# Kernel tuning notes

Hardware: AMD Instinct MI355X
Metric: run time of the kernel (lower is better)

Reference implementation:

```python
import jax, jax.numpy as jnp
import numpy as np

# dims
B, L, D0, P, K = 4, 512, 640, 128, 16
C, H, NL = 32, 4, 3            # hidden channels, heads, layers
DH = C // H
RAD_IN = P + 2                 # pair feat + bppm + distance
HPT = 0.3                      # high_prob_threshold


def _build_edges(bppm, coords):
    """Backbone + kNN + high-prob edges per sample, deduped, flattened over batch."""
    src_all, dst_all = [], []
    for b in range(B):
        s_bb = np.arange(L - 1); d_bb = np.arange(1, L)
        srcs = [s_bb, d_bb]; dsts = [d_bb, s_bb]
        c = coords[b]
        d2 = ((c[:, None, :] - c[None, :, :]) ** 2).sum(-1)
        nn = np.argsort(d2, axis=1)[:, 1:K + 1]            # exclude self
        s_knn = np.repeat(np.arange(L), K); d_knn = nn.reshape(-1)
        srcs += [s_knn, d_knn]; dsts += [d_knn, s_knn]
        iu, ju = np.triu_indices(L, 2)                      # |i-j| > 1
        m = bppm[b][iu, ju] >= HPT
        hs, hd = iu[m], ju[m]
        srcs += [hs, hd]; dsts += [hd, hs]
        e = np.unique(np.stack([np.concatenate(srcs), np.concatenate(dsts)], 1), axis=0)
        src_all.append(e[:, 0] + b * L); dst_all.append(e[:, 1] + b * L)
    return np.concatenate(src_all).astype(np.int32), np.concatenate(dst_all).astype(np.int32)


def setup_inputs() -> dict:
    rng = np.random.default_rng(0)
    sequence_rep = rng.standard_normal((B, L, D0)).astype(np.float32)
    pair_rep = rng.standard_normal((B, L, L, P)).astype(np.float32)
    u = rng.random((B, L, L)).astype(np.float32)
    bppm = (0.5 * (u + u.transpose(0, 2, 1))) ** 8          # sparse-ish symmetric BPPM
    initial_coords = (10.0 * rng.standard_normal((B, L, 3))).astype(np.float32)
    edge_src, edge_dst = _build_edges(bppm, initial_coords)

    def w(*shape):
        fan = shape[-2] if len(shape) >= 2 else shape[-1]
        return (rng.standard_normal(shape) / np.sqrt(fan)).astype(np.float32)

    inp = dict(
        sequence_rep=jnp.asarray(sequence_rep), pair_rep=jnp.asarray(pair_rep),
        bppm=jnp.asarray(bppm.astype(np.float32)), initial_coords=jnp.asarray(initial_coords),
        edge_src=jnp.asarray(edge_src), edge_dst=jnp.asarray(edge_dst),
        Win0=jnp.asarray(w(D0, C)), Win1=jnp.asarray(w(1, C)),
        Wr1=jnp.asarray(w(NL, RAD_IN, 64)), br1=jnp.zeros((NL, 64), jnp.float32),
        Wr2=jnp.asarray(w(NL, 64, 4 * C)), br2=jnp.zeros((NL, 4 * C), jnp.float32),
        Wm00=jnp.asarray(w(NL, C, C)), Wm01=jnp.asarray(w(NL, C, C)),
        Wm10=jnp.asarray(w(NL, C, C)), Wm11=jnp.asarray(w(NL, C, C)),
        Wq=jnp.asarray(w(NL, C, C)), Wself0=jnp.asarray(w(NL, C, C)), Wself1=jnp.asarray(w(NL, C, C)),
        gamma0=jnp.ones((NL, C), jnp.float32), beta0=jnp.zeros((NL, C), jnp.float32),
        gamma1=jnp.ones((NL, C), jnp.float32), Wout=jnp.asarray(w(C, 1)),
    )
    return inp


def _forward(sequence_rep, pair_rep, bppm, initial_coords,
             Win0, Win1, Wr1, br1, Wr2, br2, Wm00, Wm01, Wm10, Wm11,
             Wq, Wself0, Wself1, gamma0, beta0, gamma1, Wout, edge_src, edge_dst):
    N = B * L
    x = initial_coords.reshape(N, 3)
    h0 = sequence_rep.reshape(N, D0) @ Win0                  # [N,C] degree-0
    h1 = x[:, None, :] * Win1[0][None, :, None]              # [N,C,3] degree-1
    src, dst = edge_src, edge_dst
    rel = x[dst] - x[src]
    r = jnp.sqrt(jnp.sum(rel * rel, -1) + 1e-12)             # [E]
    rhat = rel / (r[:, None] + 1e-8)                         # Y1 spherical harmonic dir
    b_idx, si, di = src // L, src % L, dst % L
    ef = jnp.concatenate([pair_rep[b_idx, si, di], bppm[b_idx, si, di][:, None], r[:, None]], -1)

    for l in range(NL):
        rad = jax.nn.relu(ef @ Wr1[l] + br1[l]) @ Wr2[l] + br2[l]   # [E,4C] radial weights
        w00, w01, w10, w11 = jnp.split(rad, 4, axis=-1)
        h0s, h1s = h0[src], h1[src]
        dot1 = jnp.einsum('ecd,ed->ec', h1s, rhat)                  # deg1 -> deg0 path
        m0 = w00 * (h0s @ Wm00[l]) + w01 * (dot1 @ Wm01[l])          # [E,C]
        m1 = (w11[:, :, None] * jnp.einsum('ecd,cf->efd', h1s, Wm11[l])
              + (w10 * (h0s @ Wm10[l]))[:, :, None] * rhat[:, None, :])  # [E,C,3]
        # multi-head attention over incoming edges
        q = (h0 @ Wq[l]).reshape(N, H, DH)
        k = m0.reshape(-1, H, DH)
        logit = jnp.sum(q[dst] * k, -1) / np.sqrt(DH)                # [E,H]
        mx = jax.ops.segment_max(logit, dst, num_segments=N)
        mx = jnp.where(jnp.isfinite(mx), mx, 0.0)
        a = jnp.exp(logit - mx[dst])
        den = jax.ops.segment_sum(a, dst, num_segments=N)
        alpha = a / (den[dst] + 1e-9)                                # [E,H]
        agg0 = jax.ops.segment_sum(alpha[:, :, None] * k, dst, num_segments=N).reshape(N, C)
        agg1 = jax.ops.segment_sum(alpha[:, :, None, None] * m1.reshape(-1, H, DH, 3),
                                   dst, num_segments=N).reshape(N, C, 3)
        h0 = h0 + agg0 @ Wself0[l]
        h1 = h1 + jnp.einsum('ncd,cf->nfd', agg1, Wself1[l])
        # norms: LayerNorm on deg-0, equivariant norm-gating on deg-1
        mu = h0.mean(-1, keepdims=True)
        h0 = (h0 - mu) / jnp.sqrt(h0.var(-1, keepdims=True) + 1e-5) * gamma0[l] + beta0[l]
        nrm = jnp.sqrt(jnp.sum(h1 * h1, -1) + 1e-12)                 # [N,C]
        nln = (nrm - nrm.mean(-1, keepdims=True)) / jnp.sqrt(nrm.var(-1, keepdims=True) + 1e-5) * gamma1[l]
        h1 = h1 * (nln / (nrm + 1e-8))[:, :, None]
    delta = jnp.einsum('ncd,co->nod', h1, Wout)[:, 0, :]             # fiber_out {'1':1}
    return (x + delta).reshape(B, L, 3)


def reference(sequence_rep, pair_rep, bppm, initial_coords, edge_src, edge_dst,
              Win0, Win1, Wr1, br1, Wr2, br2, Wm00, Wm01, Wm10, Wm11,
              Wq, Wself0, Wself1, gamma0, beta0, gamma1, Wout):
    return _forward(sequence_rep, pair_rep, bppm, initial_coords,
                    Win0, Win1, Wr1, br1, Wr2, br2, Wm00, Wm01, Wm10, Wm11,
                    Wq, Wself0, Wself1, gamma0, beta0, gamma1, Wout, edge_src, edge_dst)
```

## Files before the change

### kernel.cpp

```cpp
#include <hip/hip_runtime.h>
#include <hip/hip_bf16.h>
#include <math.h>

#define BB 4
#define LL 512
#define D0 640
#define PP 128
#define CC 32
#define NLAYER 3
#define NN (BB*LL)
#define RADIN 130

typedef __attribute__((ext_vector_type(8))) short bf16x8;
typedef __attribute__((ext_vector_type(4))) float f32x4;

__device__ __forceinline__ short f2b(float v) {
    __hip_bfloat16 h = __float2bfloat16(v);
    short s; __builtin_memcpy(&s, &h, 2); return s;
}


__global__ void k_zero_int(int* __restrict__ p, int n) {
    int i = blockIdx.x * blockDim.x + threadIdx.x;
    if (i < n) p[i] = 0;
}

__global__ __launch_bounds__(64) void k_init_h0(const float* __restrict__ seq,
                                                const float* __restrict__ Win0,
                                                float* __restrict__ h0) {
    const int n = blockIdx.x, lane = threadIdx.x;
    const int c = lane & 31, half = lane >> 5;
    const float* s = seq + (size_t)n * D0;
    float acc = 0.f;
    const int i0 = half * (D0 / 2), i1 = i0 + (D0 / 2);
    for (int i = i0; i < i1; ++i) acc = fmaf(s[i], Win0[i * CC + c], acc);
    acc += __shfl_xor(acc, 32);
    if (lane < 32) h0[n * CC + c] = acc;
}

__global__ void k_init_h1(const float* __restrict__ x, const float* __restrict__ Win1,
                          float* __restrict__ h1) {
    int idx = blockIdx.x * blockDim.x + threadIdx.x;
    if (idx >= NN * CC) return;
    int n = idx >> 5, c = idx & 31;
    float w = Win1[c];
    const float* xp = x + n * 3;
    float* hp = h1 + (size_t)n * 96 + c * 3;
    hp[0] = xp[0] * w; hp[1] = xp[1] * w; hp[2] = xp[2] * w;
}

__global__ void k_geom(const int* __restrict__ src, const int* __restrict__ dst,
                       const float* __restrict__ x, float* __restrict__ r_e,
                       float* __restrict__ rhat, int E) {
    int e = blockIdx.x * blockDim.x + threadIdx.x;
    if (e >= E) return;
    int s = src[e], d = dst[e];
    float dx = x[d * 3 + 0] - x[s * 3 + 0];
    float dy = x[d * 3 + 1] - x[s * 3 + 1];
    float dz = x[d * 3 + 2] - x[s * 3 + 2];
    float r = sqrtf(dx * dx + dy * dy + dz * dz + 1e-12f);
    float ir = 1.f / (r + 1e-8f);
    r_e[e] = r;
    rhat[e * 3 + 0] = dx * ir; rhat[e * 3 + 1] = dy * ir; rhat[e * 3 + 2] = dz * ir;
}

__global__ void k_count(const int* __restrict__ dst, int* __restrict__ deg, int E) {
    int e = blockIdx.x * blockDim.x + threadIdx.x;
    if (e < E) atomicAdd(&deg[dst[e]], 1);
}

__global__ __launch_bounds__(64) void k_scan(const int* __restrict__ deg,
                                             int* __restrict__ rowptr,
                                             int* __restrict__ cursor) {
    const int lane = threadIdx.x;
    const int base = lane * 32;
    int loc[32]; int s = 0;
    for (int i = 0; i < 32; ++i) { loc[i] = deg[base + i]; s += loc[i]; }
    int pre = s;
    for (int off = 1; off < 64; off <<= 1) {
        int t = __shfl_up(pre, off);
        if (lane >= off) pre += t;
    }
    pre -= s;
    int run = pre;
    for (int i = 0; i < 32; ++i) { rowptr[base + i] = run; cursor[base + i] = 0; run += loc[i]; }
    if (lane == 63) rowptr[NN] = run;
}

__global__ void k_scatter(const int* __restrict__ dst, const int* __restrict__ rowptr,
                          int* __restrict__ cursor, int* __restrict__ einc, int E) {
    int e = blockIdx.x * blockDim.x + threadIdx.x;
    if (e >= E) return;
    int d = dst[e];
    int pos = atomicAdd(&cursor[d], 1);
    einc[rowptr[d] + pos] = e;
}

__global__ __launch_bounds__(256) void k_build_ef(
    const int* __restrict__ src, const int* __restrict__ dst,
    const float* __restrict__ pair, const float* __restrict__ bppm,
    const float* __restrict__ r_e, short* __restrict__ efb, int E)
{
    int e = blockIdx.x * 4 + (threadIdx.x >> 6);
    int lane = threadIdx.x & 63;
    if (e >= E) return;
    int s = src[e], d = dst[e];
    int b = s / LL, si = s % LL, di = d % LL;
    size_t prow = ((size_t)b * LL + si) * LL + di;
    const float* pr = pair + prow * PP;
    short* out = efb + (size_t)e * 160;
    out[lane] = f2b(pr[lane]);
    out[64 + lane] = f2b(pr[64 + lane]);
    if (lane < 32) {
        int idx = 128 + lane;
        float v = 0.f;
        if (idx == 128) v = bppm[prow];
        else if (idx == 129) v = r_e[e];
        out[idx] = f2b(v);
    }
}

__global__ void k_pack(const float* __restrict__ Wr1, const float* __restrict__ Wr2,
                       short* __restrict__ W1p, short* __restrict__ W2p) {
    int t = blockIdx.x * blockDim.x + threadIdx.x;
    const int tot1 = NLAYER * 5 * 4 * 64 * 8;
    const int tot2 = NLAYER * 2 * 8 * 64 * 8;
    if (t < tot1) {
        int j = t & 7; int r = t >> 3;
        int ln = r & 63; r >>= 6;
        int cb = r & 3; r >>= 2;
        int kb = r % 5; int l = r / 5;
        int row = kb * 32 + (ln >> 4) * 8 + j;
        int col = cb * 16 + (ln & 15);
        float v = (row < RADIN) ? Wr1[((size_t)l * RADIN + row) * 64 + col] : 0.f;
        W1p[t] = f2b(v);
    } else if (t < tot1 + tot2) {
        int t2 = t - tot1;
        int j = t2 & 7; int r = t2 >> 3;
        int ln = r & 63; r >>= 6;
        int cb = r & 7; r >>= 3;
        int kb = r & 1; int l = r >> 1;
        int row = kb * 32 + (ln >> 4) * 8 + j;
        int col = cb * 16 + (ln & 15);
        W2p[t2] = f2b(Wr2[((size_t)l * 64 + row) * 128 + col]);
    }
}

__global__ __launch_bounds__(256) void k_nodepre(
    int l, const float* __restrict__ h0, const float* __restrict__ h1,
    const float* __restrict__ Wq, const float* __restrict__ Wm00,
    const float* __restrict__ Wm10, const float* __restrict__ Wm11,
    float* __restrict__ qbuf, float* __restrict__ P00,
    float* __restrict__ P10, float* __restrict__ P11)
{
    __shared__ float sh0[8][32], sh1[8][96];
    const int c = threadIdx.x & 31, hw = threadIdx.x >> 5;
    const int n = blockIdx.x * 8 + hw;
    sh0[hw][c] = h0[n * CC + c];
    const float* hp = h1 + (size_t)n * 96 + c * 3;
    sh1[hw][c * 3 + 0] = hp[0]; sh1[hw][c * 3 + 1] = hp[1]; sh1[hw][c * 3 + 2] = hp[2];
    const float* WqL  = Wq   + l * 1024;
    const float* W00L = Wm00 + l * 1024;
    const float* W10L = Wm10 + l * 1024;
    const float* W11L = Wm11 + l * 1024;
    float q = 0.f, p00 = 0.f, p10 = 0.f, px = 0.f, py = 0.f, pz = 0.f;
    for (int i = 0; i < 32; ++i) {
        float a = sh0[hw][i];
        q   = fmaf(a, WqL[i * 32 + c], q);
        p00 = fmaf(a, W00L[i * 32 + c], p00);
        p10 = fmaf(a, W10L[i * 32 + c], p10);
        float w = W11L[i * 32 + c];
        px = fmaf(sh1[hw][i * 3 + 0], w, px);
        py = fmaf(sh1[hw][i * 3 + 1], w, py);
        pz = fmaf(sh1[hw][i * 3 + 2], w, pz);
    }
    qbuf[n * 32 + c] = q; P00[n * 32 + c] = p00; P10[n * 32 + c] = p10;
    float* pp = P11 + (size_t)n * 96 + c * 3;
    pp[0] = px; pp[1] = py; pp[2] = pz;
}

__global__ __launch_bounds__(256) void k_radial(
    int l, int E,
    const short* __restrict__ efb,
    const short* __restrict__ W1p,
    const short* __restrict__ W2p,
    const float* __restrict__ br1,
    const float* __restrict__ br2,
    float* __restrict__ rad)
{
    __shared__ short s_hid[4][16][72];
    const int lane = threadIdx.x & 63, wv = threadIdx.x >> 6;
    const int r16 = lane & 15, q4 = lane >> 4;
    const int e0 = blockIdx.x * 64 + wv * 16;

    f32x4 acc0 = {0.f,0.f,0.f,0.f}, acc1 = {0.f,0.f,0.f,0.f};
    f32x4 acc2 = {0.f,0.f,0.f,0.f}, acc3 = {0.f,0.f,0.f,0.f};
    int row = e0 + r16; if (row >= E) row = E - 1;
    const short* arow = efb + (size_t)row * 160 + q4 * 8;
    const short* b1b = W1p + (size_t)l * (5 * 4 * 64 * 8) + lane * 8;
    for (int kb = 0; kb < 5; ++kb) {
        bf16x8 af = *(const bf16x8*)(arow + kb * 32);
        const short* bp = b1b + kb * (4 * 64 * 8);
        bf16x8 b0 = *(const bf16x8*)(bp);
        bf16x8 b1v = *(const bf16x8*)(bp + 64 * 8);
        bf16x8 b2v = *(const bf16x8*)(bp + 2 * 64 * 8);
        bf16x8 b3v = *(const bf16x8*)(bp + 3 * 64 * 8);
        acc0 = __builtin_amdgcn_mfma_f32_16x16x32_bf16(af, b0,  acc0, 0, 0, 0);
        acc1 = __builtin_amdgcn_mfma_f32_16x16x32_bf16(af, b1v, acc1, 0, 0, 0);
        acc2 = __builtin_amdgcn_mfma_f32_16x16x32_bf16(af, b2v, acc2, 0, 0, 0);
        acc3 = __builtin_amdgcn_mfma_f32_16x16x32_bf16(af, b3v, acc3, 0, 0, 0);
    }
    {
        f32x4 a[4] = {acc0, acc1, acc2, acc3};
        for (int cb = 0; cb < 4; ++cb) {
            int col = cb * 16 + r16;
            float b = br1[l * 64 + col];
            for (int i = 0; i < 4; ++i) {
                float v = fmaxf(a[cb][i] + b, 0.f);
                s_hid[wv][q4 * 4 + i][col] = f2b(v);
            }
        }
    }
    f32x4 o[8];
    for (int cb = 0; cb < 8; ++cb) { o[cb].x=0.f; o[cb].y=0.f; o[cb].z=0.f; o[cb].w=0.f; }
    const short* b2b = W2p + (size_t)l * (2 * 8 * 64 * 8) + lane * 8;
    for (int kb = 0; kb < 2; ++kb) {
        bf16x8 af = *(const bf16x8*)(&s_hid[wv][r16][kb * 32 + q4 * 8]);
        const short* bp = b2b + kb * (8 * 64 * 8);
        for (int cb = 0; cb < 8; ++cb) {
            bf16x8 bf = *(const bf16x8*)(bp + cb * (64 * 8));
            o[cb] = __builtin_amdgcn_mfma_f32_16x16x32_bf16(af, bf, o[cb], 0, 0, 0);
        }
    }
    for (int cb = 0; cb < 8; ++cb) {
        int col = cb * 16 + r16;
        float b = br2[l * 128 + col];
        for (int i = 0; i < 4; ++i) {
            int er = e0 + q4 * 4 + i;
            if (er < E) rad[(size_t)er * 128 + col] = o[cb][i] + b;
        }
    }
}

__global__ __launch_bounds__(256) void k_edge2(
    int l, int E, const int* __restrict__ src, const float* __restrict__ rhat,
    const float* __restrict__ rad, const float* __restrict__ h1,
    const float* __restrict__ Wm01, const float* __restrict__ P00,
    const float* __restrict__ P10, const float* __restrict__ P11,
    float* __restrict__ m0buf, float* __restrict__ m1buf)
{
    __shared__ float sW[1024];
    for (int i = threadIdx.x; i < 1024; i += 256) sW[i] = Wm01[l * 1024 + i];
    __syncthreads();
    const int e = blockIdx.x * 8 + (threadIdx.x >> 5);
    if (e >= E) return;
    const int c = threadIdx.x & 31;
    const int lane = threadIdx.x & 63;
    const int base = lane & 32;
    const int s = src[e];
    float r0 = rhat[e * 3 + 0], r1 = rhat[e * 3 + 1], r2 = rhat[e * 3 + 2];
    const float* hp = h1 + (size_t)s * 96 + c * 3;
    float dot = hp[0] * r0 + hp[1] * r1 + hp[2] * r2;
    float t1 = 0.f;
    for (int i = 0; i < 32; ++i) {
        float di = __shfl(dot, base + i);
        t1 = fmaf(di, sW[i * 32 + c], t1);
    }
    const float* rp = rad + (size_t)e * 128;
    float w00 = rp[c], w01 = rp[32 + c], w10 = rp[64 + c], w11 = rp[96 + c];
    m0buf[(size_t)e * 32 + c] = fmaf(w00, P00[s * 32 + c], w01 * t1);
    float u10 = w10 * P10[s * 32 + c];
    const float* pp = P11 + (size_t)s * 96 + c * 3;
    float* mp = m1buf + (size_t)e * 96 + c * 3;
    mp[0] = fmaf(w11, pp[0], u10 * r0);
    mp[1] = fmaf(w11, pp[1], u10 * r1);
    mp[2] = fmaf(w11, pp[2], u10 * r2);
}

__global__ __launch_bounds__(64) void k_node(
    int l, const int* __restrict__ rowptr, const int* __restrict__ einc,
    const float* __restrict__ m0buf, const float* __restrict__ m1buf,
    const float* __restrict__ qbuf,
    float* __restrict__ h0, float* __restrict__ h1,
    const float* __restrict__ Ws0, const float* __restrict__ Ws1,
    const float* __restrict__ gam0, const float* __restrict__ bet0,
    const float* __restrict__ gam1)
{
    const int n = blockIdx.x, lane = threadIdx.x;
    const int c = lane & 31, half = lane >> 5;
    __shared__ float s_h0[32], s_a0[32], s_a1[96];
    if (lane < 32) s_h0[lane] = h0[n * CC + lane];
    __syncthreads();

    float qc = qbuf[n * 32 + c];

    float m_run = -INFINITY, l_run = 0.f;
    float a0 = 0.f, a1x = 0.f, a1y = 0.f, a1z = 0.f;
    const int st = rowptr[n], en = rowptr[n + 1];
    for (int i = st; i < en; i += 2) {
        const int idx = i + half;
        const bool valid = idx < en;
        float kc = 0.f, mv0 = 0.f, mv1 = 0.f, mv2 = 0.f;
        if (valid) {
            const int e = einc[idx];
            kc = m0buf[(size_t)e * 32 + c];
            const float* mp = m1buf + (size_t)e * 96 + c * 3;
            mv0 = mp[0]; mv1 = mp[1]; mv2 = mp[2];
        }
        float p = qc * kc;
        p += __shfl_xor(p, 1); p += __shfl_xor(p, 2); p += __shfl_xor(p, 4);
        if (valid) {
            float logit = p * 0.35355339059327373f;
            float mn = fmaxf(m_run, logit);
            float sc = __expf(m_run - mn);
            float w  = __expf(logit - mn);
            l_run = fmaf(l_run, sc, w);
            a0  = fmaf(a0,  sc, w * kc);
            a1x = fmaf(a1x, sc, w * mv0);
            a1y = fmaf(a1y, sc, w * mv1);
            a1z = fmaf(a1z, sc, w * mv2);
            m_run = mn;
        }
    }
    float m_o  = __shfl_xor(m_run, 32), l_o = __shfl_xor(l_run, 32);
    float a0o  = __shfl_xor(a0, 32);
    float a1xo = __shfl_xor(a1x, 32), a1yo = __shfl_xor(a1y, 32), a1zo = __shfl_xor(a1z, 32);
    float mn = fmaxf(m_run, m_o);
    float sa = 0.f, sb = 0.f;
    if (mn > -INFINITY) { sa = __expf(m_run - mn); sb = __expf(m_o - mn); }
    float den = l_run * sa + l_o * sb;
    float inv = 1.0f / (den + 1e-9f);
    float g0c = (a0  * sa + a0o  * sb) * inv;
    float g1x = (a1x * sa + a1xo * sb) * inv;
    float g1y = (a1y * sa + a1yo * sb) * inv;
    float g1z = (a1z * sa + a1zo * sb) * inv;
    if (lane < 32) {
        s_a0[c] = g0c;
        s_a1[c * 3 + 0] = g1x; s_a1[c * 3 + 1] = g1y; s_a1[c * 3 + 2] = g1z;
    }
    __syncthreads();

    float x0 = s_h0[c];
    {
        const float* W = Ws0 + l * 1024;
        for (int i = 0; i < 32; ++i) x0 = fmaf(s_a0[i], W[i * 32 + c], x0);
    }
    float mu = x0;
    mu += __shfl_xor(mu, 1); mu += __shfl_xor(mu, 2); mu += __shfl_xor(mu, 4);
    mu += __shfl_xor(mu, 8); mu += __shfl_xor(mu, 16);
    mu *= (1.f / 32.f);
    float sq = x0 * x0;
    sq += __shfl_xor(sq, 1); sq += __shfl_xor(sq, 2); sq += __shfl_xor(sq, 4);
    sq += __shfl_xor(sq, 8); sq += __shfl_xor(sq, 16);
    float var = sq * (1.f / 32.f) - mu * mu;
    float h0n = (x0 - mu) * rsqrtf(var + 1e-5f) * gam0[l * 32 + c] + bet0[l * 32 + c];
    if (lane < 32) h0[n * CC + c] = h0n;

    const float* hp = h1 + (size_t)n * 96 + c * 3;
    float v0 = hp[0], v1 = hp[1], v2 = hp[2];
    {
        const float* W = Ws1 + l * 1024;
        for (int i = 0; i < 32; ++i) {
            float w = W[i * 32 + c];
            v0 = fmaf(s_a1[i * 3 + 0], w, v0);
            v1 = fmaf(s_a1[i * 3 + 1], w, v1);
            v2 = fmaf(s_a1[i * 3 + 2], w, v2);
        }
    }
    float nrm = sqrtf(v0 * v0 + v1 * v1 + v2 * v2 + 1e-12f);
    float mu2 = nrm;
    mu2 += __shfl_xor(mu2, 1); mu2 += __shfl_xor(mu2, 2); mu2 += __shfl_xor(mu2, 4);
    mu2 += __shfl_xor(mu2, 8); mu2 += __shfl_xor(mu2, 16);
    mu2 *= (1.f / 32.f);
    float sq2 = nrm * nrm;
    sq2 += __shfl_xor(sq2, 1); sq2 += __shfl_xor(sq2, 2); sq2 += __shfl_xor(sq2, 4);
    sq2 += __shfl_xor(sq2, 8); sq2 += __shfl_xor(sq2, 16);
    float var2 = sq2 * (1.f / 32.f) - mu2 * mu2;
    float nln = (nrm - mu2) * rsqrtf(var2 + 1e-5f) * gam1[l * 32 + c];
    float scl = nln / (nrm + 1e-8f);
    if (lane < 32) {
        float* hw = h1 + (size_t)n * 96 + c * 3;
        hw[0] = v0 * scl; hw[1] = v1 * scl; hw[2] = v2 * scl;
    }
}

__global__ void k_out(const float* __restrict__ x, const float* __restrict__ h1,
                      const float* __restrict__ Wout, float* __restrict__ out) {
    int idx = blockIdx.x * blockDim.x + threadIdx.x;
    if (idx >= NN * 3) return;
    int n = idx / 3, d = idx % 3;
    float acc = x[idx];
    const float* hp = h1 + (size_t)n * 96 + d;
    for (int cc = 0; cc < 32; ++cc) acc = fmaf(hp[cc * 3], Wout[cc], acc);
    out[idx] = acc;
}

extern "C" void kernel_launch(void* const* d_in, const int* in_sizes, int n_in,
                              void* d_out, int out_size, void* d_ws, size_t ws_size,
                              hipStream_t stream) {
    const float* seq  = (const float*)d_in[0];
    const float* pair = (const float*)d_in[1];
    const float* bppm = (const float*)d_in[2];
    const float* x    = (const float*)d_in[3];
    const int*   src  = (const int*)d_in[4];
    const int*   dst  = (const int*)d_in[5];
    const float* Win0 = (const float*)d_in[6];
    const float* Win1 = (const float*)d_in[7];
    const float* Wr1  = (const float*)d_in[8];
    const float* br1  = (const float*)d_in[9];
    const float* Wr2  = (const float*)d_in[10];
    const float* br2  = (const float*)d_in[11];
    const float* Wm00 = (const float*)d_in[12];
    const float* Wm01 = (const float*)d_in[13];
    const float* Wm10 = (const float*)d_in[14];
    const float* Wm11 = (const float*)d_in[15];
    const float* Wq   = (const float*)d_in[16];
    const float* Ws0  = (const float*)d_in[17];
    const float* Ws1  = (const float*)d_in[18];
    const float* gam0 = (const float*)d_in[19];
    const float* bet0 = (const float*)d_in[20];
    const float* gam1 = (const float*)d_in[21];
    const float* Wout = (const float*)d_in[22];
    const int E = in_sizes[4];

    char* w = (char*)d_ws;
    auto alloc = [&](size_t nbytes) {
        void* p = (void*)w;
        w += (nbytes + 255) & ~(size_t)255;
        return p;
    };
    float* h0    = (float*)alloc((size_t)NN * CC * 4);
    float* h1    = (float*)alloc((size_t)NN * CC * 3 * 4);
    float* r_e   = (float*)alloc((size_t)E * 4);
    float* rhat  = (float*)alloc((size_t)E * 3 * 4);
    float* m0buf = (float*)alloc((size_t)E * CC * 4);
    float* m1buf = (float*)alloc((size_t)E * CC * 3 * 4);
    int* deg     = (int*)alloc((size_t)NN * 4);
    int* rowptr  = (int*)alloc((size_t)(NN + 1) * 4);
    int* cursor  = (int*)alloc((size_t)NN * 4);
    int* einc    = (int*)alloc((size_t)E * 4);
    short* efb   = (short*)alloc((size_t)E * 160 * 2);
    short* W1p   = (short*)alloc((size_t)NLAYER * 5 * 4 * 64 * 8 * 2);
    short* W2p   = (short*)alloc((size_t)NLAYER * 2 * 8 * 64 * 8 * 2);
    float* rad   = (float*)alloc((size_t)E * 128 * 4);
    float* qbuf  = (float*)alloc((size_t)NN * 32 * 4);
    float* P00   = (float*)alloc((size_t)NN * 32 * 4);
    float* P10   = (float*)alloc((size_t)NN * 32 * 4);
    float* P11   = (float*)alloc((size_t)NN * 96 * 4);

    const int TB = 256;
    k_zero_int<<<(NN + TB - 1) / TB, TB, 0, stream>>>(deg, NN);
    k_init_h0<<<NN, 64, 0, stream>>>(seq, Win0, h0);
    k_init_h1<<<(NN * CC + TB - 1) / TB, TB, 0, stream>>>(x, Win1, h1);
    k_geom<<<(E + TB - 1) / TB, TB, 0, stream>>>(src, dst, x, r_e, rhat, E);
    k_count<<<(E + TB - 1) / TB, TB, 0, stream>>>(dst, deg, E);
    k_scan<<<1, 64, 0, stream>>>(deg, rowptr, cursor);
    k_scatter<<<(E + TB - 1) / TB, TB, 0, stream>>>(dst, rowptr, cursor, einc, E);
    k_build_ef<<<(E + 3) / 4, 256, 0, stream>>>(src, dst, pair, bppm, r_e, efb, E);
    {
        int tot = NLAYER * 5 * 4 * 64 * 8 + NLAYER * 2 * 8 * 64 * 8;
        k_pack<<<(tot + TB - 1) / TB, TB, 0, stream>>>(Wr1, Wr2, W1p, W2p);
    }

    for (int l = 0; l < NLAYER; ++l) {
        k_nodepre<<<NN / 8, 256, 0, stream>>>(l, h0, h1, Wq, Wm00, Wm10, Wm11,
                                              qbuf, P00, P10, P11);
        k_radial<<<(E + 63) / 64, 256, 0, stream>>>(l, E, efb, W1p, W2p, br1, br2, rad);
        k_edge2<<<(E + 7) / 8, 256, 0, stream>>>(l, E, src, rhat, rad, h1, Wm01,
                                                 P00, P10, P11, m0buf, m1buf);
        k_node<<<NN, 64, 0, stream>>>(l, rowptr, einc, m0buf, m1buf, qbuf, h0, h1,
                                      Ws0, Ws1, gam0, bet0, gam1);
    }
    k_out<<<(NN * 3 + TB - 1) / TB, TB, 0, stream>>>(x, h1, Wout, (float*)d_out);
}
```

Before: 904.3 us.

## Fuse radial MLP with edge message kernel and write messages in CSR order

Merges the radial-MLP kernel and the edge message kernel into one, so the per-edge 128-wide radial weights stay in shared memory instead of going through a global buffer. Edge messages are written to a single interleaved 128-float row at each edge's destination-sorted position, using a precomputed permutation. The node kernel then reads messages contiguously without the einc indirection. The cost is more shared memory per block (about 40KB), which may lower occupancy, and scattered writes from the edge kernel.

```diff
diff --git a/kernel.cpp b/kernel.cpp
--- a/kernel.cpp
+++ b/kernel.cpp
@@ -88,12 +88,12 @@
 }
 
 __global__ void k_scatter(const int* __restrict__ dst, const int* __restrict__ rowptr,
-                          int* __restrict__ cursor, int* __restrict__ einc, int E) {
+                          int* __restrict__ cursor, int* __restrict__ eperm, int E) {
     int e = blockIdx.x * blockDim.x + threadIdx.x;
     if (e >= E) return;
     int d = dst[e];
     int pos = atomicAdd(&cursor[d], 1);
-    einc[rowptr[d] + pos] = e;
+    eperm[e] = rowptr[d] + pos;
 }
 
 __global__ __launch_bounds__(256) void k_build_ef(
@@ -179,19 +179,32 @@
     pp[0] = px; pp[1] = py; pp[2] = pz;
 }
 
-__global__ __launch_bounds__(256) void k_radial(
+__global__ __launch_bounds__(256) void k_radedge(
     int l, int E,
+    const int* __restrict__ src,
+    const float* __restrict__ rhat,
     const short* __restrict__ efb,
     const short* __restrict__ W1p,
     const short* __restrict__ W2p,
     const float* __restrict__ br1,
     const float* __restrict__ br2,
-    float* __restrict__ rad)
+    const float* __restrict__ Wm01,
+    const float* __restrict__ h1,
+    const float* __restrict__ P00,
+    const float* __restrict__ P10,
+    const float* __restrict__ P11,
+    const int* __restrict__ eperm,
+    float* __restrict__ mbuf)
 {
     __shared__ short s_hid[4][16][72];
+    __shared__ float s_rad[64][132];
+    __shared__ float sW[1024];
     const int lane = threadIdx.x & 63, wv = threadIdx.x >> 6;
     const int r16 = lane & 15, q4 = lane >> 4;
-    const int e0 = blockIdx.x * 64 + wv * 16;
+    const int eb = blockIdx.x * 64;
+    const int e0 = eb + wv * 16;
+
+    for (int i = threadIdx.x; i < 1024; i += 256) sW[i] = Wm01[l * 1024 + i];
 
     f32x4 acc0 = {0.f,0.f,0.f,0.f}, acc1 = {0.f,0.f,0.f,0.f};
     f32x4 acc2 = {0.f,0.f,0.f,0.f}, acc3 = {0.f,0.f,0.f,0.f};
@@ -236,50 +249,43 @@
         int col = cb * 16 + r16;
         float b = br2[l * 128 + col];
         for (int i = 0; i < 4; ++i) {
-            int er = e0 + q4 * 4 + i;
-            if (er < E) rad[(size_t)er * 128 + col] = o[cb][i] + b;
-        }
-    }
-}
-
-__global__ __launch_bounds__(256) void k_edge2(
-    int l, int E, const int* __restrict__ src, const float* __restrict__ rhat,
-    const float* __restrict__ rad, const float* __restrict__ h1,
-    const float* __restrict__ Wm01, const float* __restrict__ P00,
-    const float* __restrict__ P10, const float* __restrict__ P11,
-    float* __restrict__ m0buf, float* __restrict__ m1buf)
-{
-    __shared__ float sW[1024];
-    for (int i = threadIdx.x; i < 1024; i += 256) sW[i] = Wm01[l * 1024 + i];
+            s_rad[wv * 16 + q4 * 4 + i][col] = o[cb][i] + b;
+        }
+    }
     __syncthreads();
-    const int e = blockIdx.x * 8 + (threadIdx.x >> 5);
-    if (e >= E) return;
-    const int c = threadIdx.x & 31;
-    const int lane = threadIdx.x & 63;
+
+    const int hw = threadIdx.x >> 5;
+    const int c = lane & 31;
     const int base = lane & 32;
-    const int s = src[e];
-    float r0 = rhat[e * 3 + 0], r1 = rhat[e * 3 + 1], r2 = rhat[e * 3 + 2];
-    const float* hp = h1 + (size_t)s * 96 + c * 3;
-    float dot = hp[0] * r0 + hp[1] * r1 + hp[2] * r2;
-    float t1 = 0.f;
-    for (int i = 0; i < 32; ++i) {
-        float di = __shfl(dot, base + i);
-        t1 = fmaf(di, sW[i * 32 + c], t1);
-    }
-    const float* rp = rad + (size_t)e * 128;
-    float w00 = rp[c], w01 = rp[32 + c], w10 = rp[64 + c], w11 = rp[96 + c];
-    m0buf[(size_t)e * 32 + c] = fmaf(w00, P00[s * 32 + c], w01 * t1);
-    float u10 = w10 * P10[s * 32 + c];
-    const float* pp = P11 + (size_t)s * 96 + c * 3;
-    float* mp = m1buf + (size_t)e * 96 + c * 3;
-    mp[0] = fmaf(w11, pp[0], u10 * r0);
-    mp[1] = fmaf(w11, pp[1], u10 * r1);
-    mp[2] = fmaf(w11, pp[2], u10 * r2);
+    for (int it = 0; it < 8; ++it) {
+        const int el = hw * 8 + it;
+        const int e = eb + el;
+        if (e >= E) break;
+        const int s = src[e];
+        const float r0 = rhat[e * 3 + 0], r1 = rhat[e * 3 + 1], r2 = rhat[e * 3 + 2];
+        const float* hp = h1 + (size_t)s * 96 + c * 3;
+        const float dot = hp[0] * r0 + hp[1] * r1 + hp[2] * r2;
+        float t1 = 0.f;
+        for (int i = 0; i < 32; ++i) {
+            float di = __shfl(dot, base + i);
+            t1 = fmaf(di, sW[i * 32 + c], t1);
+        }
+        const float w00 = s_rad[el][c],      w01 = s_rad[el][32 + c];
+        const float w10 = s_rad[el][64 + c], w11 = s_rad[el][96 + c];
+        const float m0 = fmaf(w00, P00[s * 32 + c], w01 * t1);
+        const float u10 = w10 * P10[s * 32 + c];
+        const float* pp = P11 + (size_t)s * 96 + c * 3;
+        float* mp = mbuf + (size_t)eperm[e] * 128;
+        mp[c] = m0;
+        mp[32 + c * 3 + 0] = fmaf(w11, pp[0], u10 * r0);
+        mp[32 + c * 3 + 1] = fmaf(w11, pp[1], u10 * r1);
+        mp[32 + c * 3 + 2] = fmaf(w11, pp[2], u10 * r2);
+    }
 }
 
 __global__ __launch_bounds__(64) void k_node(
-    int l, const int* __restrict__ rowptr, const int* __restrict__ einc,
-    const float* __restrict__ m0buf, const float* __restrict__ m1buf,
+    int l, const int* __restrict__ rowptr,
+    const float* __restrict__ mbuf,
     const float* __restrict__ qbuf,
     float* __restrict__ h0, float* __restrict__ h1,
     const float* __restrict__ Ws0, const float* __restrict__ Ws1,
@@ -302,10 +308,11 @@
         const bool valid = idx < en;
         float kc = 0.f, mv0 = 0.f, mv1 = 0.f, mv2 = 0.f;
         if (valid) {
-            const int e = einc[idx];
-            kc = m0buf[(size_t)e * 32 + c];
-            const float* mp = m1buf + (size_t)e * 96 + c * 3;
-            mv0 = mp[0]; mv1 = mp[1]; mv2 = mp[2];
+            const float* row = mbuf + (size_t)idx * 128;
+            kc = row[c];
+            mv0 = row[32 + c * 3 + 0];
+            mv1 = row[32 + c * 3 + 1];
+            mv2 = row[32 + c * 3 + 2];
         }
         float p = qc * kc;
         p += __shfl_xor(p, 1); p += __shfl_xor(p, 2); p += __shfl_xor(p, 4);
@@ -433,16 +440,14 @@
     float* h1    = (float*)alloc((size_t)NN * CC * 3 * 4);
     float* r_e   = (float*)alloc((size_t)E * 4);
     float* rhat  = (float*)alloc((size_t)E * 3 * 4);
-    float* m0buf = (float*)alloc((size_t)E * CC * 4);
-    float* m1buf = (float*)alloc((size_t)E * CC * 3 * 4);
+    float* mbuf  = (float*)alloc((size_t)E * 128 * 4);
     int* deg     = (int*)alloc((size_t)NN * 4);
     int* rowptr  = (int*)alloc((size_t)(NN + 1) * 4);
     int* cursor  = (int*)alloc((size_t)NN * 4);
-    int* einc    = (int*)alloc((size_t)E * 4);
+    int* eperm   = (int*)alloc((size_t)E * 4);
     short* efb   = (short*)alloc((size_t)E * 160 * 2);
     short* W1p   = (short*)alloc((size_t)NLAYER * 5 * 4 * 64 * 8 * 2);
     short* W2p   = (short*)alloc((size_t)NLAYER * 2 * 8 * 64 * 8 * 2);
-    float* rad   = (float*)alloc((size_t)E * 128 * 4);
     float* qbuf  = (float*)alloc((size_t)NN * 32 * 4);
     float* P00   = (float*)alloc((size_t)NN * 32 * 4);
     float* P10   = (float*)alloc((size_t)NN * 32 * 4);
@@ -455,7 +460,7 @@
     k_geom<<<(E + TB - 1) / TB, TB, 0, stream>>>(src, dst, x, r_e, rhat, E);
     k_count<<<(E + TB - 1) / TB, TB, 0, stream>>>(dst, deg, E);
     k_scan<<<1, 64, 0, stream>>>(deg, rowptr, cursor);
-    k_scatter<<<(E + TB - 1) / TB, TB, 0, stream>>>(dst, rowptr, cursor, einc, E);
+    k_scatter<<<(E + TB - 1) / TB, TB, 0, stream>>>(dst, rowptr, cursor, eperm, E);
     k_build_ef<<<(E + 3) / 4, 256, 0, stream>>>(src, dst, pair, bppm, r_e, efb, E);
     {
         int tot = NLAYER * 5 * 4 * 64 * 8 + NLAYER * 2 * 8 * 64 * 8;
@@ -465,10 +470,10 @@
     for (int l = 0; l < NLAYER; ++l) {
         k_nodepre<<<NN / 8, 256, 0, stream>>>(l, h0, h1, Wq, Wm00, Wm10, Wm11,
                                               qbuf, P00, P10, P11);
-        k_radial<<<(E + 63) / 64, 256, 0, stream>>>(l, E, efb, W1p, W2p, br1, br2, rad);
-        k_edge2<<<(E + 7) / 8, 256, 0, stream>>>(l, E, src, rhat, rad, h1, Wm01,
-                                                 P00, P10, P11, m0buf, m1buf);
-        k_node<<<NN, 64, 0, stream>>>(l, rowptr, einc, m0buf, m1buf, qbuf, h0, h1,
+        k_radedge<<<(E + 63) / 64, 256, 0, stream>>>(l, E, src, rhat, efb, W1p, W2p,
+                                                     br1, br2, Wm01, h1,
+                                                     P00, P10, P11, eperm, mbuf);
+        k_node<<<NN, 64, 0, stream>>>(l, rowptr, mbuf, qbuf, h0, h1,
                                       Ws0, Ws1, gam0, bet0, gam1);
     }
     k_out<<<(NN * 3 + TB - 1) / TB, TB, 0, stream>>>(x, h1, Wout, (float*)d_out);
```

Measured after the change: 855.7 us. 5.4% less time.
